# Kernel tuning notes

Measured on AMD Instinct MI355X. Metric: run time of the kernel, lower is better.

## Reference

```python
import jax, jax.numpy as jnp
import numpy as np

A, D, TOTAL = 1024, 128, 524288


def setup_inputs() -> dict:
    key = jax.random.key(0)
    k1, k2, k3 = jax.random.split(key, 3)
    anchors = jax.random.normal(k1, (A, D), dtype=jnp.float32)
    Xn_flat = jax.random.normal(k2, (TOTAL, D), dtype=jnp.float32)
    segment_ids = jnp.sort(jax.random.randint(k3, (TOTAL,), 0, A))
    return {"anchors": anchors, "Xn_flat": Xn_flat, "segment_ids": segment_ids}


def reference(anchors, Xn_flat, segment_ids):
    # anchors: [A, D]; Xn_flat: [TOTAL, D] (ragged segments flattened);
    # segment_ids: [TOTAL] row -> anchor index (sorted).
    d_feat = anchors.shape[1]
    eps = 1e-4 / d_feat  # eps = 0.0001 / x1.size(0), x1 = anchor vector of size D
    # L2dist(p=2, squared=False): sqrt(sum(|x1-x2|^2, dim=1) + eps)
    diff = jnp.abs(Xn_flat - anchors[segment_ids])          # [TOTAL, D]
    sq_dist = jnp.sum(diff * diff, axis=1)                  # [TOTAL]
    dist = jnp.sqrt(sq_dist + eps)                          # [TOTAL]
    # per-anchor sum of distances, then log1p, accumulated over anchors
    per_anchor = jax.ops.segment_sum(dist, segment_ids, num_segments=anchors.shape[0])  # [A]
    intra_class_dist = jnp.sum(jnp.log1p(per_anchor))
    n_total = Xn_flat.shape[0]  # N = sum of segment lengths
    return intra_class_dist / n_total
```

## Files before the change

kernel.cpp:

```cpp
#include <hip/hip_runtime.h>
#include <math.h>

#define DFEAT 128
#define A_MAX 1024
#define ROWS_PER_BLOCK 64

__global__ __launch_bounds__(256) void icc_dist_kernel(
    const float* __restrict__ anchors,
    const float* __restrict__ Xn,
    const int*   __restrict__ seg,
    float*       __restrict__ per_anchor,
    int total, int num_anchors)
{
    __shared__ float acc[A_MAX];
    const int tid = threadIdx.x;
    for (int i = tid; i < A_MAX; i += 256) acc[i] = 0.0f;
    __syncthreads();

    const int lane = tid & 31;
    const int hw   = tid >> 5;
    const int rowBase = blockIdx.x * ROWS_PER_BLOCK;
    const float eps = 1e-4f / (float)DFEAT;

    #pragma unroll
    for (int r = 0; r < ROWS_PER_BLOCK / 8; ++r) {
        const int row = rowBase + r * 8 + hw;
        if (row < total) {
            const int a = seg[row];
            const float4 x  = *reinterpret_cast<const float4*>(
                Xn + (size_t)row * DFEAT + lane * 4);
            const float4 av = *reinterpret_cast<const float4*>(
                anchors + (size_t)a * DFEAT + lane * 4);
            const float dx = x.x - av.x;
            const float dy = x.y - av.y;
            const float dz = x.z - av.z;
            const float dw = x.w - av.w;
            float sq = dx * dx + dy * dy + dz * dz + dw * dw;
            #pragma unroll
            for (int off = 16; off > 0; off >>= 1)
                sq += __shfl_down(sq, off, 32);
            if (lane == 0) {
                const float dist = sqrtf(sq + eps);
                if (a < A_MAX) atomicAdd(&acc[a], dist);
                else           atomicAdd(&per_anchor[a], dist);
            }
        }
    }
    __syncthreads();
    for (int i = tid; i < num_anchors && i < A_MAX; i += 256) {
        const float v = acc[i];
        if (v != 0.0f) atomicAdd(&per_anchor[i], v);
    }
}

__global__ __launch_bounds__(256) void icc_final_kernel(
    const float* __restrict__ per_anchor,
    float*       __restrict__ out,
    int num_anchors, float inv_total)
{
    __shared__ float red[4];
    const int tid = threadIdx.x;
    float s = 0.0f;
    for (int i = tid; i < num_anchors; i += 256)
        s += log1pf(per_anchor[i]);
    #pragma unroll
    for (int off = 32; off > 0; off >>= 1)
        s += __shfl_down(s, off, 64);
    if ((tid & 63) == 0) red[tid >> 6] = s;
    __syncthreads();
    if (tid == 0) {
        const float t = red[0] + red[1] + red[2] + red[3];
        out[0] = t * inv_total;
    }
}

extern "C" void kernel_launch(void* const* d_in, const int* in_sizes, int n_in,
                              void* d_out, int out_size, void* d_ws, size_t ws_size,
                              hipStream_t stream) {
    const float* anchors = (const float*)d_in[0];
    const float* Xn      = (const float*)d_in[1];
    const int*   seg     = (const int*)d_in[2];
    float* out = (float*)d_out;

    const int num_anchors = in_sizes[0] / DFEAT;
    const int total       = in_sizes[2];

    float* per_anchor = (float*)d_ws;
    hipMemsetAsync(per_anchor, 0, (size_t)num_anchors * sizeof(float), stream);

    const int blocks = (total + ROWS_PER_BLOCK - 1) / ROWS_PER_BLOCK;
    icc_dist_kernel<<<blocks, 256, 0, stream>>>(
        anchors, Xn, seg, per_anchor, total, num_anchors);
    icc_final_kernel<<<1, 256, 0, stream>>>(
        per_anchor, out, num_anchors, 1.0f / (float)total);
}
```

Before: 361.3 us.

## Compute segment offsets and process one anchor per block with fused log1p reduction

Adds a pass that derives segment start offsets from the sorted segment ids. The distance kernel then runs one block per anchor, loading the anchor vector once and reducing distances in registers. The final log1p and sum are fused into that kernel through a single atomic on the output. This removes the per-row anchor gathers, the shared-memory atomics and the separate final kernel. In exchange, the grid shrinks to 1024 blocks with uneven segment lengths, which risks lower memory-level parallelism and load imbalance, and the result becomes nondeterministic in summation order.

```diff
diff --git a/kernel.cpp b/kernel.cpp
--- a/kernel.cpp
+++ b/kernel.cpp
@@ -2,75 +2,61 @@
 #include <math.h>
 
 #define DFEAT 128
-#define A_MAX 1024
-#define ROWS_PER_BLOCK 64
 
-__global__ __launch_bounds__(256) void icc_dist_kernel(
+__global__ __launch_bounds__(256) void seg_bounds_kernel(
+    const int* __restrict__ seg, int* __restrict__ offs, int total, int A)
+{
+    const int i = blockIdx.x * 256 + threadIdx.x;
+    if (i >= total) return;
+    const int s = seg[i];
+    const int p = (i == 0) ? -1 : seg[i - 1];
+    for (int a = p + 1; a <= s; ++a) offs[a] = i;
+    if (i == total - 1)
+        for (int a = s + 1; a <= A; ++a) offs[a] = total;
+}
+
+__global__ __launch_bounds__(256) void icc_anchor_kernel(
     const float* __restrict__ anchors,
     const float* __restrict__ Xn,
-    const int*   __restrict__ seg,
-    float*       __restrict__ per_anchor,
-    int total, int num_anchors)
+    const int*   __restrict__ offs,
+    float*       __restrict__ out,
+    float inv_total)
 {
-    __shared__ float acc[A_MAX];
-    const int tid = threadIdx.x;
-    for (int i = tid; i < A_MAX; i += 256) acc[i] = 0.0f;
-    __syncthreads();
-
+    const int a    = blockIdx.x;
+    const int tid  = threadIdx.x;
     const int lane = tid & 31;
     const int hw   = tid >> 5;
-    const int rowBase = blockIdx.x * ROWS_PER_BLOCK;
     const float eps = 1e-4f / (float)DFEAT;
 
-    #pragma unroll
-    for (int r = 0; r < ROWS_PER_BLOCK / 8; ++r) {
-        const int row = rowBase + r * 8 + hw;
-        if (row < total) {
-            const int a = seg[row];
-            const float4 x  = *reinterpret_cast<const float4*>(
-                Xn + (size_t)row * DFEAT + lane * 4);
-            const float4 av = *reinterpret_cast<const float4*>(
-                anchors + (size_t)a * DFEAT + lane * 4);
-            const float dx = x.x - av.x;
-            const float dy = x.y - av.y;
-            const float dz = x.z - av.z;
-            const float dw = x.w - av.w;
-            float sq = dx * dx + dy * dy + dz * dz + dw * dw;
-            #pragma unroll
-            for (int off = 16; off > 0; off >>= 1)
-                sq += __shfl_down(sq, off, 32);
-            if (lane == 0) {
-                const float dist = sqrtf(sq + eps);
-                if (a < A_MAX) atomicAdd(&acc[a], dist);
-                else           atomicAdd(&per_anchor[a], dist);
-            }
-        }
+    const int lo = offs[a];
+    const int hi = offs[a + 1];
+
+    const float4 av = *reinterpret_cast<const float4*>(
+        anchors + (size_t)a * DFEAT + lane * 4);
+
+    float dsum = 0.0f;
+    for (int row = lo + hw; row < hi; row += 8) {
+        const float4 x = *reinterpret_cast<const float4*>(
+            Xn + (size_t)row * DFEAT + lane * 4);
+        const float dx = x.x - av.x;
+        const float dy = x.y - av.y;
+        const float dz = x.z - av.z;
+        const float dw = x.w - av.w;
+        float sq = dx * dx + dy * dy + dz * dz + dw * dw;
+        #pragma unroll
+        for (int off = 16; off > 0; off >>= 1)
+            sq += __shfl_down(sq, off, 32);
+        if (lane == 0) dsum += sqrtf(sq + eps);
     }
-    __syncthreads();
-    for (int i = tid; i < num_anchors && i < A_MAX; i += 256) {
-        const float v = acc[i];
-        if (v != 0.0f) atomicAdd(&per_anchor[i], v);
-    }
-}
 
-__global__ __launch_bounds__(256) void icc_final_kernel(
-    const float* __restrict__ per_anchor,
-    float*       __restrict__ out,
-    int num_anchors, float inv_total)
-{
-    __shared__ float red[4];
-    const int tid = threadIdx.x;
-    float s = 0.0f;
-    for (int i = tid; i < num_anchors; i += 256)
-        s += log1pf(per_anchor[i]);
-    #pragma unroll
-    for (int off = 32; off > 0; off >>= 1)
-        s += __shfl_down(s, off, 64);
-    if ((tid & 63) == 0) red[tid >> 6] = s;
+    __shared__ float part[8];
+    if (lane == 0) part[hw] = dsum;
     __syncthreads();
     if (tid == 0) {
-        const float t = red[0] + red[1] + red[2] + red[3];
-        out[0] = t * inv_total;
+        float s = 0.0f;
+        #pragma unroll
+        for (int h = 0; h < 8; ++h) s += part[h];
+        atomicAdd(out, log1pf(s) * inv_total);
     }
 }
 
@@ -82,15 +68,13 @@
     const int*   seg     = (const int*)d_in[2];
     float* out = (float*)d_out;
 
-    const int num_anchors = in_sizes[0] / DFEAT;
-    const int total       = in_sizes[2];
+    const int A     = in_sizes[0] / DFEAT;
+    const int total = in_sizes[2];
 
-    float* per_anchor = (float*)d_ws;
-    hipMemsetAsync(per_anchor, 0, (size_t)num_anchors * sizeof(float), stream);
+    int* offs = (int*)d_ws;
 
-    const int blocks = (total + ROWS_PER_BLOCK - 1) / ROWS_PER_BLOCK;
-    icc_dist_kernel<<<blocks, 256, 0, stream>>>(
-        anchors, Xn, seg, per_anchor, total, num_anchors);
-    icc_final_kernel<<<1, 256, 0, stream>>>(
-        per_anchor, out, num_anchors, 1.0f / (float)total);
+    hipMemsetAsync(out, 0, sizeof(float), stream);
+    seg_bounds_kernel<<<(total + 255) / 256, 256, 0, stream>>>(seg, offs, total, A);
+    icc_anchor_kernel<<<A, 256, 0, stream>>>(anchors, Xn, offs, out,
+                                             1.0f / (float)total);
 }
```

Result: slower. 377.2 us (+4.4%).
